# Optimization experiments

Hardware: AMD Instinct MI355X
Metric: run time of the kernel (lower is better)

## Reference

```python
import jax, jax.numpy as jnp
import numpy as np

DIM = 96
RES = (8, 56, 56)
WIN = (8, 7, 7)
SHIFT = (4, 3, 3)
HEADS = (3, 6)
EPS = 1e-5


def _rel_pos_index(wd, wh, ww):
    coords = np.stack(np.meshgrid(np.arange(wd), np.arange(wh), np.arange(ww), indexing='ij'))
    cf = coords.reshape(3, -1)                       # (3, N)
    rel = (cf[:, :, None] - cf[:, None, :]).transpose(1, 2, 0)  # (N, N, 3)
    rel[..., 0] += wd - 1
    rel[..., 1] += wh - 1
    rel[..., 2] += ww - 1
    rel[..., 0] *= (2 * wh - 1) * (2 * ww - 1)
    rel[..., 1] *= (2 * ww - 1)
    return rel.sum(-1)                               # (N, N) int


def _attn_mask(D, H, W, win, shift):
    wd, wh, ww = win
    sd, sh, sw = shift
    img = np.zeros((D, H, W), np.float32)
    cnt = 0
    for ds in (slice(0, -wd), slice(-wd, -sd), slice(-sd, None)):
        for hs in (slice(0, -wh), slice(-wh, -sh), slice(-sh, None)):
            for vs in (slice(0, -ww), slice(-ww, -sw), slice(-sw, None)):
                img[ds, hs, vs] = cnt
                cnt += 1
    m = img.reshape(D // wd, wd, H // wh, wh, W // ww, ww)
    m = m.transpose(0, 2, 4, 1, 3, 5).reshape(-1, wd * wh * ww)   # (nW, N)
    diff = m[:, None, :] - m[:, :, None]
    return np.where(diff != 0, np.float32(-100.0), np.float32(0.0))


def _ln_c(x, w, b):
    # LayerNorm over the channel dim of (B,C,D,H,W)
    mu = x.mean(axis=1, keepdims=True)
    var = ((x - mu) ** 2).mean(axis=1, keepdims=True)
    xn = (x - mu) * jax.lax.rsqrt(var + EPS)
    return xn * w[None, :, None, None, None] + b[None, :, None, None, None]


def _window_partition(x, win):
    B, C, D, H, W = x.shape
    wd, wh, ww = win
    x = x.transpose(0, 2, 3, 4, 1)
    x = x.reshape(B, D // wd, wd, H // wh, wh, W // ww, ww, C)
    x = x.transpose(0, 1, 3, 5, 2, 4, 6, 7)
    return x.reshape(-1, wd * wh * ww, C)            # (B*nW, N, C)


def _window_reverse(w, win, B, D, H, W):
    wd, wh, ww = win
    C = w.shape[-1]
    x = w.reshape(B, D // wd, H // wh, W // ww, wd, wh, ww, C)
    x = x.transpose(0, 1, 4, 2, 5, 3, 6, 7).reshape(B, D, H, W, C)
    return x.transpose(0, 4, 1, 2, 3)


def _win_attn(xw, mask, rel_idx, qkv_w, qkv_b, proj_w, proj_b, rpb, h):
    Bn, N, C = xw.shape
    dh = C // h
    qkv = (xw @ qkv_w.T + qkv_b).reshape(Bn, N, 3, h, dh).transpose(2, 0, 3, 1, 4)
    q, k, v = qkv[0], qkv[1], qkv[2]                 # (Bn, h, N, dh)
    attn = jnp.einsum('bhnd,bhmd->bhnm', q * (dh ** -0.5), k)
    bias = rpb[rel_idx.reshape(-1)].reshape(N, N, h).transpose(2, 0, 1)
    attn = attn + bias[None]
    nW = mask.shape[0]
    attn = (attn.reshape(Bn // nW, nW, h, N, N) + mask[None, :, None]).reshape(Bn, h, N, N)
    attn = jax.nn.softmax(attn, axis=-1)
    out = jnp.einsum('bhnm,bhmd->bhnd', attn, v).transpose(0, 2, 1, 3).reshape(Bn, N, C)
    return out @ proj_w.T + proj_b


def _conv3d(x, w, b, groups=1):
    y = jax.lax.conv_general_dilated(x, w, (1, 1, 1), 'SAME',
                                     dimension_numbers=('NCDHW', 'OIDHW', 'NCDHW'),
                                     feature_group_count=groups)
    return y + b[None, :, None, None, None]


def setup_inputs() -> dict:
    key = jax.random.key(0)
    ks = jax.random.split(key, 16)
    C = DIM
    s = 0.02
    inp = {
        'x': jax.random.normal(ks[0], (2, C, *RES), jnp.float32),
        'ln1_w': jnp.ones((C,), jnp.float32), 'ln1_b': jnp.zeros((C,), jnp.float32),
        'ln2_w': jnp.ones((C,), jnp.float32), 'ln2_b': jnp.zeros((C,), jnp.float32),
        'qkv_w0': jax.random.normal(ks[1], (3 * C, C), jnp.float32) * s,
        'qkv_b0': jnp.zeros((3 * C,), jnp.float32),
        'proj_w0': jax.random.normal(ks[2], (C, C), jnp.float32) * s,
        'proj_b0': jnp.zeros((C,), jnp.float32),
        'rpb0': jax.random.normal(ks[3], (15 * 13 * 13, HEADS[0]), jnp.float32) * s,
        'qkv_w1': jax.random.normal(ks[4], (3 * C, C), jnp.float32) * s,
        'qkv_b1': jnp.zeros((3 * C,), jnp.float32),
        'proj_w1': jax.random.normal(ks[5], (C, C), jnp.float32) * s,
        'proj_b1': jnp.zeros((C,), jnp.float32),
        'rpb1': jax.random.normal(ks[6], (15 * 13 * 13, HEADS[1]), jnp.float32) * s,
        'alpha_attn': jax.random.normal(ks[7], (2,), jnp.float32),
        'conv3_w': jax.random.normal(ks[8], (C, C, 3, 3, 3), jnp.float32) * s,
        'conv3_b': jnp.zeros((C,), jnp.float32),
        'conv1_w': jax.random.normal(ks[9], (C, C, 1, 1, 1), jnp.float32) * s,
        'conv1_b': jnp.zeros((C,), jnp.float32),
        'dw_w': jax.random.normal(ks[10], (C, 1, 3, 3, 3), jnp.float32) * s,
        'dw_b': jnp.zeros((C,), jnp.float32),
        'alpha_ffn': jax.random.normal(ks[11], (4,), jnp.float32),
    }
    return inp


def reference(x, ln1_w, ln1_b, ln2_w, ln2_b,
              qkv_w0, qkv_b0, proj_w0, proj_b0, rpb0,
              qkv_w1, qkv_b1, proj_w1, proj_b1, rpb1,
              alpha_attn, conv3_w, conv3_b, conv1_w, conv1_b, dw_w, dw_b, alpha_ffn):
    B, C, D, H, W = x.shape
    sd, sh, sw = SHIFT
    mask = jnp.asarray(_attn_mask(D, H, W, WIN, SHIFT))     # (nW, N, N), constant
    rel_idx = jnp.asarray(_rel_pos_index(*WIN))             # (N, N), constant

    # --- attention branch (soft NAS mixture) ---
    xn = _ln_c(x, ln1_w, ln1_b)
    shifted = jnp.roll(xn, (-sd, -sh, -sw), axis=(2, 3, 4))
    win = _window_partition(shifted, WIN)
    aw = jax.nn.softmax(alpha_attn)
    a0 = _win_attn(win, mask, rel_idx, qkv_w0, qkv_b0, proj_w0, proj_b0, rpb0, HEADS[0])
    a1 = _win_attn(win, mask, rel_idx, qkv_w1, qkv_b1, proj_w1, proj_b1, rpb1, HEADS[1])
    attn_out = aw[0] * a0 + aw[1] * a1
    xr = _window_reverse(attn_out, WIN, B, D, H, W)
    x_attn = jnp.roll(xr, (sd, sh, sw), axis=(2, 3, 4))
    x1 = x + x_attn                                         # gate=None -> 1.0, drop_path=0

    # --- FFN branch (soft NAS mixture of conv ops) ---
    x2 = _ln_c(x1, ln2_w, ln2_b)
    fw = jax.nn.softmax(alpha_ffn)
    ffn = (fw[0] * _conv3d(x2, conv3_w, conv3_b)
           + fw[1] * _conv3d(x2, conv1_w, conv1_b)
           + fw[2] * _conv3d(x2, dw_w, dw_b, groups=C)
           + fw[3] * x2)
    return x1 + ffn
```

## Files before the change

kernel.cpp:

```cpp
#include <hip/hip_runtime.h>

#define NWIN 128
#define NTOK 392
#define SPAT 25088
#define NELEM 4816896

typedef unsigned short u16t;
typedef unsigned int u32t;
typedef __attribute__((ext_vector_type(8))) short short8;
typedef __attribute__((ext_vector_type(4))) float f32x4;

#define PW 58
#define PHW 3364
#define PSPAT 33640
#define XPAD_U16 6458880
#define WCOMB_N 248832
#define WPROJ_N 18432
#define NTOKTOT 50176
#define LOG2E 1.44269504f

__device__ __forceinline__ unsigned int f2bf(float f) {
  unsigned int u = __float_as_uint(f);
  return (u + 0x7fffu + ((u >> 16) & 1u)) >> 16;
}
__device__ __forceinline__ unsigned int pack2(float a, float b) {
  return f2bf(a) | (f2bf(b) << 16);
}
__device__ __forceinline__ u32t cvtpk(float lo, float hi) {
  u32t r;
  asm("v_cvt_pk_bf16_f32 %0, %1, %2" : "=v"(r) : "v"(lo), "v"(hi));
  return r;
}
__device__ __forceinline__ float exp2v(float x) {
  return __builtin_amdgcn_exp2f(x);
}
__device__ __forceinline__ float bflo(unsigned int u) { return __uint_as_float(u << 16); }

__global__ __launch_bounds__(128)
void k_ln1_win(const float* __restrict__ x, const float* __restrict__ lw,
               const float* __restrict__ lb, u16t* __restrict__ xw) {
  __shared__ float s1[128], s2[128];
  int t = blockIdx.x;
  int win = t / NTOK, n = t % NTOK;
  int b = win >> 6, wrem = win & 63;
  int hwin = wrem >> 3, wwin = wrem & 7;
  int ld = n / 49, r = n % 49, lh = r / 7, lw2 = r % 7;
  int d = (ld + 4) & 7;
  int h = (hwin * 7 + lh + 3) % 56;
  int w = (wwin * 7 + lw2 + 3) % 56;
  size_t base = (size_t)b * 96 * SPAT + d * 3136 + h * 56 + w;
  int c = threadIdx.x;
  float v = (c < 96) ? x[base + (size_t)c * SPAT] : 0.f;
  s1[c] = v; s2[c] = v * v;
  __syncthreads();
  #pragma unroll
  for (int st = 64; st > 0; st >>= 1) {
    if (c < st) { s1[c] += s1[c + st]; s2[c] += s2[c + st]; }
    __syncthreads();
  }
  float mu = s1[0] * (1.f / 96.f);
  float var = s2[0] * (1.f / 96.f) - mu * mu;
  float rs = rsqrtf(var + 1e-5f);
  if (c < 96) xw[(size_t)t * 96 + c] = (u16t)f2bf((v - mu) * rs * lw[c] + lb[c]);
}

__global__ __launch_bounds__(256)
void k_qprep(const float* __restrict__ w0, const float* __restrict__ w1,
             u16t* __restrict__ wq) {
  int e = blockIdx.x * 256 + threadIdx.x;
  if (e >= 2 * 27648) return;
  wq[e] = (u16t)f2bf(e < 27648 ? w0[e] : w1[e - 27648]);
}

template<int DH>
__global__ __launch_bounds__(256)
void k_qkv_mfma(const u16t* __restrict__ xw, const u16t* __restrict__ wq,
                const float* __restrict__ bias, u16t* __restrict__ qkvh) {
  int tid = threadIdx.x;
  int lane = tid & 63, wv = tid >> 6;
  int c = lane & 15, lg = lane >> 4;
  int t = blockIdx.x * 64 + wv * 16 + c;
  const u16t* bp = xw + (size_t)t * 96 + lg * 8;
  short8 bv[3];
  #pragma unroll
  for (int kc = 0; kc < 3; ++kc)
    bv[kc] = *reinterpret_cast<const short8*>(bp + kc * 32);
  f32x4 acc[18];
  #pragma unroll
  for (int f = 0; f < 18; ++f) acc[f] = (f32x4){0.f, 0.f, 0.f, 0.f};
  #pragma unroll
  for (int kc = 0; kc < 3; ++kc) {
    #pragma unroll
    for (int f = 0; f < 18; ++f) {
      short8 av = *reinterpret_cast<const short8*>(
          wq + (size_t)(f * 16 + c) * 96 + kc * 32 + lg * 8);
      acc[f] = __builtin_amdgcn_mfma_f32_16x16x32_bf16(av, bv[kc], acc[f], 0, 0, 0);
    }
  }
  #pragma unroll
  for (int f = 0; f < 18; ++f) {
    int co = f * 16 + lg * 4;
    float4 bb = *reinterpret_cast<const float4*>(bias + co);
    uint2 st = make_uint2(pack2(acc[f][0] + bb.x, acc[f][1] + bb.y),
                          pack2(acc[f][2] + bb.z, acc[f][3] + bb.w));
    int sel = co / 96, rem = co % 96;
    int head = rem / DH, dh = rem % DH;
    *reinterpret_cast<uint2*>(qkvh + (size_t)sel * NTOKTOT * 96
        + (size_t)head * NTOKTOT * DH + (size_t)t * DH + dh) = st;
  }
}

template<int H>
__global__ __launch_bounds__(256)
void k_rprep(const float* __restrict__ rpb, u16t* __restrict__ rpbc) {
  int e = blockIdx.x * 256 + threadIdx.x;
  if (e >= H * 2536) return;
  int h = e / 2536, idx = e % 2536;
  rpbc[e] = (idx < 2535) ? (u16t)f2bf(rpb[idx * H + h] * LOG2E) : (u16t)0;
}

template<int H, int DH>
__global__ __launch_bounds__(512, (DH == 16) ? 6 : 4)
void k_attn_mfma(const u16t* __restrict__ qkvh, const u16t* __restrict__ rpbc,
                 u16t* __restrict__ aout) {
  constexpr float SCALE2 = ((DH == 32) ? 0.17677669529663689f : 0.25f) * LOG2E;
  constexpr float MASKV = -100.f * LOG2E;
  constexpr float THR = 8.f * LOG2E;
  constexpr int NT = DH / 16;
  constexpr int QSPLIT = (DH == 16) ? 1 : 2;
  constexpr int KROW = (DH == 32) ? 32 : 16;
  constexpr int KS_U16 = (DH == 32) ? (416 * 32) : (417 * 16);
  constexpr int BLK = 512;
  __shared__ __align__(16) u16t Ks[KS_U16];
  __shared__ __align__(16) u16t VTs[DH * 424];
  __shared__ u16t rpbs[2536];
  __shared__ u16t Ts[416];
  __shared__ u32t RGp[104];
  __shared__ u32t RGm[26];

  int bid = blockIdx.x;
  int xcd = bid & 7, i = bid >> 3;
  int win = xcd * 16 + (i & 15);
  int hp = i >> 4;
  int head = (DH == 32) ? (hp >> 1) : hp;
  int part = (DH == 32) ? (hp & 1) : 0;
  int wrem = win & 63;
  int hwin = wrem >> 3, wwin = wrem & 7;
  int tid = threadIdx.x;
  int lane = tid & 63, wv = tid >> 6;
  int c = lane & 15, lg = lane >> 4;

  const u16t* qh = qkvh + (size_t)head * NTOKTOT * DH + (size_t)win * NTOK * DH;
  const u16t* kh = qh + (size_t)NTOKTOT * 96;
  const u16t* vh = qh + (size_t)2 * NTOKTOT * 96;
  u16t* ao = aout + (size_t)head * NTOKTOT * DH + (size_t)win * NTOK * DH;

  {
    uint4 z = make_uint4(0u, 0u, 0u, 0u);
    uint4* k4 = (uint4*)Ks;
    for (int i2 = tid; i2 < KS_U16 / 8; i2 += BLK) k4[i2] = z;
    uint4* v4 = (uint4*)VTs;
    for (int i2 = tid; i2 < (DH * 424) / 8; i2 += BLK) v4[i2] = z;
  }
  __syncthreads();
  constexpr int DG = DH / 8;
  for (int u = tid; u < NTOK * DG; u += BLK) {
    int j = u / DG, dg = u % DG;
    uint4 kv = *reinterpret_cast<const uint4*>(kh + (size_t)j * DH + dg * 8);
    int sch = (DH == 32) ? (dg ^ (j & 3)) : (dg ^ ((j & 1) ^ ((j >> 2) & 1)));
    *reinterpret_cast<uint4*>(&Ks[j * KROW + sch * 8]) = kv;
    union { uint4 q; u16t s[8]; } vv;
    vv.q = *reinterpret_cast<const uint4*>(vh + (size_t)j * DH + dg * 8);
    #pragma unroll
    for (int ee = 0; ee < 8; ++ee) VTs[(dg * 8 + ee) * 424 + j] = vv.s[ee];
  }
  for (int i2 = tid; i2 < 2536; i2 += BLK) rpbs[i2] = rpbc[head * 2536 + i2];
  for (int j = tid; j < 416; j += BLK) {
    u16t tv = 0;
    if (j < NTOK) {
      int ld = j / 49, r = j % 49, lh = r / 7, lw = r % 7;
      tv = (u16t)(ld * 169 + lh * 13 + lw);
    }
    Ts[j] = tv;
  }
  for (int j4 = tid; j4 < 104; j4 += BLK) {
    u32t w = 0;
    #pragma unroll
    for (int bb = 0; bb < 4; ++bb) {
      int j = j4 * 4 + bb;
      u32t rg = 255;
      if (j < NTOK) {
        int ld = j / 49, r = j % 49, lh = r / 7, lw = r % 7;
        int hpp = hwin * 7 + lh, wpp = wwin * 7 + lw;
        int rd = (ld < 4) ? 1 : 2;
        int rh = (hpp < 49) ? 0 : ((hpp < 53) ? 1 : 2);
        int rw = (wpp < 49) ? 0 : ((wpp < 53) ? 1 : 2);
        rg = (u32t)(rd * 9 + rh * 3 + rw);
      }
      w |= rg << (8 * bb);
    }
    RGp[j4] = w;
  }
  __syncthreads();
  if (tid < 26) {
    u32t msk = 0;
    #pragma unroll
    for (int j4 = 0; j4 < 4; ++j4) {
      u32t w = RGp[tid * 4 + j4];
      #pragma unroll
      for (int bb = 0; bb < 4; ++bb) {
        u32t rg = (w >> (8 * bb)) & 255u;
        if (rg < 27u) msk |= (1u << rg);
      }
    }
    RGm[tid] = msk;
  }
  __syncthreads();

  constexpr int QBASE = 25 / QSPLIT;
  constexpr int QREM = 25 % QSPLIT;
  int q0 = part * QBASE + ((part < QREM) ? part : QREM);
  int q1 = q0 + QBASE + ((part < QREM) ? 1 : 0);

  for (int qt = q0 + wv; qt < q1; qt += 8) {
    int qtok = qt * 16 + c;
    int qcl = (qtok < NTOK) ? qtok : NTOK - 1;
    int Tq = (int)Ts[qcl] + 1267;
    u32t rgq = (RGp[qcl >> 2] >> ((qcl & 3) * 8)) & 255u;
    u32t qmask = RGm[qt < 25 ? qt : 24];
    short8 bq;
    {
      const u16t* qp = qh + (size_t)qcl * DH;
      union { u32t u[4]; short8 v; } bu;
      #pragma unroll
      for (int i2 = 0; i2 < 4; ++i2) {
        u16t e0 = (DH == 32 || lg < 2) ? qp[lg * 8 + 2 * i2] : (u16t)0;
        u16t e1 = (DH == 32 || lg < 2) ? qp[lg * 8 + 2 * i2 + 1] : (u16t)0;
        bu.u[i2] = (u32t)e0 | ((u32t)e1 << 16);
      }
      bq = bu.v;
    }
    float m = -1e30f, lsum = 0.f;
    f32x4 oacc[NT];
    #pragma unroll
    for (int ot = 0; ot < NT; ++ot) oacc[ot] = (f32x4){0.f, 0.f, 0.f, 0.f};
    int srcl = ((lane >> 4) & 1) * 32 + c;
    #pragma unroll 1
    for (int tt = 0; tt < 13; ++tt) {
      u32t kmask = RGm[2 * tt] | ((2 * tt + 1 < 26) ? RGm[2 * tt + 1] : 0u);
      if ((qmask & kmask) == 0u) continue;
      f32x4 p0, p1;
      #pragma unroll
      for (int half = 0; half < 2; ++half) {
        int t = 2 * tt + half;
        int addr;
        if (DH == 32) {
          addr = (16 * t + c) * 32 + ((lg ^ (c & 3)) * 8);
        } else {
          int fc = (c & 1) ^ ((c >> 2) & 1);
          addr = (lg < 2) ? ((16 * t + c) * 16 + (((lg & 1) ^ fc) * 8)) : (416 * 16);
        }
        short8 av = *reinterpret_cast<const short8*>(&Ks[addr]);
        f32x4 a = (f32x4){0.f, 0.f, 0.f, 0.f};
        a = __builtin_amdgcn_mfma_f32_16x16x32_bf16(av, bq, a, 0, 0, 0);
        int kb = 16 * t + lg * 4;
        const u32t* tsp = reinterpret_cast<const u32t*>(&Ts[kb]);
        u32t tsa = tsp[0], tsb = tsp[1];
        u32t rgw = RGp[4 * t + lg];
        f32x4 p;
        p[0] = a[0] * SCALE2 + bflo((u32t)rpbs[Tq - (int)(tsa & 0xffffu)])
             + ((((rgw      ) & 255u) != rgq) ? MASKV : 0.f);
        p[1] = a[1] * SCALE2 + bflo((u32t)rpbs[Tq - (int)(tsa >> 16)])
             + ((((rgw >>  8) & 255u) != rgq) ? MASKV : 0.f);
        p[2] = a[2] * SCALE2 + bflo((u32t)rpbs[Tq - (int)(tsb & 0xffffu)])
             + ((((rgw >> 16) & 255u) != rgq) ? MASKV : 0.f);
        p[3] = a[3] * SCALE2 + bflo((u32t)rpbs[Tq - (int)(tsb >> 16)])
             + ((((rgw >> 24)        ) != rgq) ? MASKV : 0.f);
        if (half == 0) p0 = p; else p1 = p;
      }
      float pm = fmaxf(fmaxf(fmaxf(p0[0], p0[1]), fmaxf(p0[2], p0[3])),
                       fmaxf(fmaxf(p1[0], p1[1]), fmaxf(p1[2], p1[3])));
      pm = fmaxf(pm, __shfl_xor(pm, 16));
      pm = fmaxf(pm, __shfl_xor(pm, 32));
      bool dead = (pm <= m - 25.f) || (pm <= -90.f);
      if (__all(dead)) continue;
      if (!__all(pm <= m + THR)) {
        float mnew = fmaxf(pm, m);
        float fac = exp2v(m - mnew);
        lsum *= fac;
        #pragma unroll
        for (int ot = 0; ot < NT; ++ot) oacc[ot] *= fac;
        m = mnew;
      }
      #pragma unroll
      for (int j = 0; j < 4; ++j) {
        p0[j] = exp2v(p0[j] - m);
        p1[j] = exp2v(p1[j] - m);
      }
      lsum += p0[0] + p0[1] + p0[2] + p0[3] + p1[0] + p1[1] + p1[2] + p1[3];
      u32t pk0x = cvtpk(p0[0], p0[1]);
      u32t pk0y = cvtpk(p0[2], p0[3]);
      u32t pk1x = cvtpk(p1[0], p1[1]);
      u32t pk1y = cvtpk(p1[2], p1[3]);
      u32t ax = (u32t)__shfl((int)pk0x, srcl),      ay = (u32t)__shfl((int)pk0y, srcl);
      u32t bx = (u32t)__shfl((int)pk0x, srcl + 16), by = (u32t)__shfl((int)pk0y, srcl + 16);
      u32t cx = (u32t)__shfl((int)pk1x, srcl),      cy = (u32t)__shfl((int)pk1y, srcl);
      u32t dx = (u32t)__shfl((int)pk1x, srcl + 16), dy = (u32t)__shfl((int)pk1y, srcl + 16);
      bool hi = (lane & 32) != 0;
      union { u32t u[4]; short8 v; } au;
      au.u[0] = hi ? cx : ax; au.u[1] = hi ? cy : ay;
      au.u[2] = hi ? dx : bx; au.u[3] = hi ? dy : by;
      #pragma unroll
      for (int ot = 0; ot < NT; ++ot) {
        short8 bv = *reinterpret_cast<const short8*>(
            &VTs[(ot * 16 + c) * 424 + 32 * tt + lg * 8]);
        oacc[ot] = __builtin_amdgcn_mfma_f32_16x16x32_bf16(au.v, bv, oacc[ot], 0, 0, 0);
      }
    }
    lsum += __shfl_xor(lsum, 16);
    lsum += __shfl_xor(lsum, 32);
    float inv = 1.f / lsum;
    float invj[4];
    #pragma unroll
    for (int j = 0; j < 4; ++j) invj[j] = __shfl(inv, lg * 4 + j);
    #pragma unroll
    for (int j = 0; j < 4; ++j) {
      int q = qt * 16 + lg * 4 + j;
      if (q < NTOK) {
        #pragma unroll
        for (int ot = 0; ot < NT; ++ot)
          ao[(size_t)q * DH + ot * 16 + c] = (u16t)f2bf(oacc[ot][j] * invj[j]);
      }
    }
  }
}

__global__ __launch_bounds__(256)
void k_pprep(const float* __restrict__ pw0, const float* __restrict__ pb0,
             const float* __restrict__ pw1, const float* __restrict__ pb1,
             const float* __restrict__ alpha,
             u16t* __restrict__ wp, float* __restrict__ bp) {
  int e = blockIdx.x * 256 + threadIdx.x;
  if (e >= WPROJ_N) return;
  float al0 = alpha[0], al1 = alpha[1];
  float m = fmaxf(al0, al1);
  float e0 = expf(al0 - m), e1 = expf(al1 - m);
  float aw0 = e0 / (e0 + e1), aw1 = e1 / (e0 + e1);
  int co = e / 192, k = e % 192;
  float v = (k < 96) ? aw0 * pw0[co * 96 + k] : aw1 * pw1[co * 96 + k - 96];
  wp[e] = (u16t)f2bf(v);
  if (e < 96) bp[e] = aw0 * pb0[e] + aw1 * pb1[e];
}

__global__ __launch_bounds__(64)
void k_proj_mfma(const u16t* __restrict__ a0, const u16t* __restrict__ a1,
                 const u16t* __restrict__ wp, const float* __restrict__ bp,
                 const float* __restrict__ x, float* __restrict__ x1) {
  int lane = threadIdx.x;
  int c = lane & 15, lg = lane >> 4;
  int t = blockIdx.x * 16 + c;
  int win = t / NTOK, n = t % NTOK;
  int b = win >> 6, wrem = win & 63;
  int hwin = wrem >> 3, wwin = wrem & 7;
  int ld = n / 49, r = n % 49, lh = r / 7, lw = r % 7;
  int d = (ld + 4) & 7;
  int h = (hwin * 7 + lh + 3) % 56;
  int w = (wwin * 7 + lw + 3) % 56;
  size_t base = (size_t)b * 96 * SPAT + d * 3136 + h * 56 + w;

  f32x4 acc[6];
  #pragma unroll
  for (int f = 0; f < 6; ++f) acc[f] = (f32x4){0.f, 0.f, 0.f, 0.f};
  #pragma unroll
  for (int kc = 0; kc < 6; ++kc) {
    short8 bv;
    if (kc < 3) {
      bv = *reinterpret_cast<const short8*>(a0 + ((size_t)kc * NTOKTOT + t) * 32 + lg * 8);
    } else {
      int h1 = (kc - 3) * 2 + (lg >> 1);
      bv = *reinterpret_cast<const short8*>(a1 + ((size_t)h1 * NTOKTOT + t) * 16 + (lg & 1) * 8);
    }
    #pragma unroll
    for (int f = 0; f < 6; ++f) {
      short8 av = *reinterpret_cast<const short8*>(wp + (f * 16 + c) * 192 + kc * 32 + lg * 8);
      acc[f] = __builtin_amdgcn_mfma_f32_16x16x32_bf16(av, bv, acc[f], 0, 0, 0);
    }
  }
  #pragma unroll
  for (int f = 0; f < 6; ++f) {
    #pragma unroll
    for (int j = 0; j < 4; ++j) {
      int co = f * 16 + lg * 4 + j;
      size_t idx = base + (size_t)co * SPAT;
      x1[idx] = x[idx] + acc[f][j] + bp[co];
    }
  }
}

__global__ __launch_bounds__(256)
void k_zero(uint4* __restrict__ p, int n) {
  int i = blockIdx.x * 256 + threadIdx.x;
  if (i < n) p[i] = make_uint4(0u, 0u, 0u, 0u);
}

__global__ __launch_bounds__(256)
void k_wprep(const float* __restrict__ c3w, const float* __restrict__ c3b,
             const float* __restrict__ c1w, const float* __restrict__ c1b,
             const float* __restrict__ dww, const float* __restrict__ dwb,
             const float* __restrict__ alpha,
             u16t* __restrict__ wcomb, float* __restrict__ bcomb) {
  int e = blockIdx.x * 256 + threadIdx.x;
  if (e >= WCOMB_N) return;
  float a0 = alpha[0], a1 = alpha[1], a2 = alpha[2], a3 = alpha[3];
  float mx = fmaxf(fmaxf(a0, a1), fmaxf(a2, a3));
  float e0 = expf(a0 - mx), e1 = expf(a1 - mx), e2 = expf(a2 - mx), e3 = expf(a3 - mx);
  float inv = 1.f / (e0 + e1 + e2 + e3);
  float f0 = e0 * inv, f1 = e1 * inv, f2 = e2 * inv, f3 = e3 * inv;
  int ko = e / 9216, rm = e % 9216, co = rm / 96, ci = rm % 96;
  float v = f0 * c3w[(co * 96 + ci) * 27 + ko];
  if (ko == 13) v += f1 * c1w[co * 96 + ci];
  if (ci == co) v += f2 * dww[co * 27 + ko];
  if (ko == 13 && ci == co) v += f3;
  wcomb[e] = (u16t)f2bf(v);
  if (e < 96) bcomb[e] = f0 * c3b[e] + f1 * c1b[e] + f2 * dwb[e];
}

__global__ __launch_bounds__(256)
void k_ln2pad(const float* __restrict__ x1, const float* __restrict__ lw,
              const float* __restrict__ lb, u16t* __restrict__ xpad) {
  int p = blockIdx.x * 256 + threadIdx.x;
  int b = p / SPAT, s = p % SPAT;
  int d = s / 3136, r = s % 3136, h = r / 56, w = r % 56;
  const float* xp = x1 + (size_t)b * 96 * SPAT + s;
  float sum = 0.f, sq = 0.f;
  #pragma unroll 8
  for (int c = 0; c < 96; ++c) {
    float v = xp[(size_t)c * SPAT];
    sum += v; sq += v * v;
  }
  float mu = sum * (1.f / 96.f);
  float var = sq * (1.f / 96.f) - mu * mu;
  float rs = rsqrtf(var + 1e-5f);
  int psp = ((b * 10 + d + 1) * 58 + (h + 1)) * 58 + (w + 1);
  u16t* op = xpad + (size_t)psp * 96;
  #pragma unroll
  for (int g = 0; g < 12; ++g) {
    float v0 = xp[(size_t)(8 * g + 0) * SPAT], v1 = xp[(size_t)(8 * g + 1) * SPAT];
    float v2 = xp[(size_t)(8 * g + 2) * SPAT], v3 = xp[(size_t)(8 * g + 3) * SPAT];
    float v4 = xp[(size_t)(8 * g + 4) * SPAT], v5 = xp[(size_t)(8 * g + 5) * SPAT];
    float v6 = xp[(size_t)(8 * g + 6) * SPAT], v7 = xp[(size_t)(8 * g + 7) * SPAT];
    uint4 st;
    st.x = pack2((v0 - mu) * rs * lw[8*g+0] + lb[8*g+0], (v1 - mu) * rs * lw[8*g+1] + lb[8*g+1]);
    st.y = pack2((v2 - mu) * rs * lw[8*g+2] + lb[8*g+2], (v3 - mu) * rs * lw[8*g+3] + lb[8*g+3]);
    st.z = pack2((v4 - mu) * rs * lw[8*g+4] + lb[8*g+4], (v5 - mu) * rs * lw[8*g+5] + lb[8*g+5]);
    st.w = pack2((v6 - mu) * rs * lw[8*g+6] + lb[8*g+6], (v7 - mu) * rs * lw[8*g+7] + lb[8*g+7]);
    *reinterpret_cast<uint4*>(op + g * 8) = st;
  }
}

__global__ __launch_bounds__(256)
void k_ffn_mfma(const u16t* __restrict__ xpad, const u16t* __restrict__ wcomb,
                const float* __restrict__ bcomb, float* __restrict__ out) {
  __shared__ __align__(16) u16t wls[2][48 * 104];
  int tid = threadIdx.x;
  int lane = tid & 63, wv = tid >> 6;
  int c = lane & 15, kg = lane >> 4;
  int bid = blockIdx.x;
  int coh = bid & 1;
  int sp = bid >> 1;
  int swz = (sp & 7) * 98 + (sp >> 3);
  int m = swz * 64 + wv * 16 + c;
  int b = m / SPAT, r = m % SPAT;
  int d = r / 3136, r2 = r % 3136, h = r2 / 56, w = r2 % 56;
  int psp0 = ((b * 10 + d) * 58 + h) * 58 + w;
  int pbase = psp0 * 96 + kg * 8;
  int obase = b * (96 * SPAT) + r;

  f32x4 acc[3];
  #pragma unroll
  for (int ff = 0; ff < 3; ++ff) acc[ff] = (f32x4){0.f, 0.f, 0.f, 0.f};

  {
    const uint4* src = (const uint4*)(wcomb) + coh * 576;
    for (int e = tid; e < 576; e += 256) {
      uint4 v = src[e];
      int lco = (e * 8) / 96, ci = (e * 8) % 96;
      *reinterpret_cast<uint4*>(&wls[0][lco * 104 + ci]) = v;
    }
  }
  __syncthreads();
  int buf = 0;
  for (int ko = 0; ko < 27; ++ko) {
    int kd = ko / 9, kh = (ko / 3) % 3, kw = ko % 3;
    int tapoff = (kd * PHW + kh * PW + kw) * 96;
    if (ko + 1 < 27) {
      const uint4* src = (const uint4*)(wcomb) + (ko + 1) * 1152 + coh * 576;
      for (int e = tid; e < 576; e += 256) {
        uint4 v = src[e];
        int lco = (e * 8) / 96, ci = (e * 8) % 96;
        *reinterpret_cast<uint4*>(&wls[buf ^ 1][lco * 104 + ci]) = v;
      }
    }
    #pragma unroll
    for (int cc = 0; cc < 3; ++cc) {
      short8 bv = *reinterpret_cast<const short8*>(xpad + pbase + tapoff + cc * 32);
      #pragma unroll
      for (int ff = 0; ff < 3; ++ff) {
        short8 av = *reinterpret_cast<const short8*>(
            &wls[buf][(ff * 16 + c) * 104 + cc * 32 + kg * 8]);
        acc[ff] = __builtin_amdgcn_mfma_f32_16x16x32_bf16(av, bv, acc[ff], 0, 0, 0);
      }
    }
    __syncthreads();
    buf ^= 1;
  }
  #pragma unroll
  for (int ff = 0; ff < 3; ++ff)
    #pragma unroll
    for (int j = 0; j < 4; ++j) {
      int co = coh * 48 + ff * 16 + kg * 4 + j;
      float* o = out + obase + co * SPAT;
      *o = *o + acc[ff][j] + bcomb[co];
    }
}

extern "C" void kernel_launch(void* const* d_in, const int* in_sizes, int n_in,
                              void* d_out, int out_size, void* d_ws, size_t ws_size,
                              hipStream_t stream) {
  (void)in_sizes; (void)n_in; (void)out_size; (void)ws_size;
  const float* x      = (const float*)d_in[0];
  const float* ln1w   = (const float*)d_in[1];
  const float* ln1b   = (const float*)d_in[2];
  const float* ln2w   = (const float*)d_in[3];
  const float* ln2b   = (const float*)d_in[4];
  const float* qkvw0  = (const float*)d_in[5];
  const float* qkvb0  = (const float*)d_in[6];
  const float* projw0 = (const float*)d_in[7];
  const float* projb0 = (const float*)d_in[8];
  const float* rpb0   = (const float*)d_in[9];
  const float* qkvw1  = (const float*)d_in[10];
  const float* qkvb1  = (const float*)d_in[11];
  const float* projw1 = (const float*)d_in[12];
  const float* projb1 = (const float*)d_in[13];
  const float* rpb1   = (const float*)d_in[14];
  const float* aattn  = (const float*)d_in[15];
  const float* c3w    = (const float*)d_in[16];
  const float* c3b    = (const float*)d_in[17];
  const float* c1w    = (const float*)d_in[18];
  const float* c1b    = (const float*)d_in[19];
  const float* dww    = (const float*)d_in[20];
  const float* dwb    = (const float*)d_in[21];
  const float* affn   = (const float*)d_in[22];

  u16t* u    = (u16t*)d_ws;
  u16t* xw   = u;
  u16t* a0   = xw + (size_t)NTOKTOT * 96;
  u16t* a1   = a0 + (size_t)3 * NTOKTOT * 32;
  u16t* qkvh = a1 + (size_t)6 * NTOKTOT * 16;
  u16t* wq   = qkvh + (size_t)3 * NTOKTOT * 96;
  u16t* rpbc0 = wq + 2 * 27648;
  u16t* rpbc1 = rpbc0 + 3 * 2536;
  u16t* xpad  = qkvh;
  u16t* wcomb = xpad + XPAD_U16;
  float* bcomb = (float*)(wcomb + WCOMB_N);
  u16t* wproj = (u16t*)(bcomb + 96);
  float* bproj = (float*)(wproj + WPROJ_N);
  float* x1  = (float*)d_out;

  k_ln1_win<<<NWIN * NTOK, 128, 0, stream>>>(x, ln1w, ln1b, xw);
  k_qprep<<<216, 256, 0, stream>>>(qkvw0, qkvw1, wq);
  k_rprep<3><<<30, 256, 0, stream>>>(rpb0, rpbc0);
  k_rprep<6><<<60, 256, 0, stream>>>(rpb1, rpbc1);
  k_qkv_mfma<32><<<784, 256, 0, stream>>>(xw, wq, qkvb0, qkvh);
  k_attn_mfma<3, 32><<<768, 512, 0, stream>>>(qkvh, rpbc0, a0);
  k_qkv_mfma<16><<<784, 256, 0, stream>>>(xw, wq + 27648, qkvb1, qkvh);
  k_attn_mfma<6, 16><<<768, 512, 0, stream>>>(qkvh, rpbc1, a1);
  k_zero<<<(XPAD_U16 / 8 + 255) / 256, 256, 0, stream>>>((uint4*)xpad, XPAD_U16 / 8);
  k_wprep<<<(WCOMB_N + 255) / 256, 256, 0, stream>>>(c3w, c3b, c1w, c1b, dww, dwb,
                                                     affn, wcomb, bcomb);
  k_pprep<<<(WPROJ_N + 255) / 256, 256, 0, stream>>>(projw0, projb0, projw1, projb1,
                                                     aattn, wproj, bproj);
  k_proj_mfma<<<3136, 64, 0, stream>>>(a0, a1, wproj, bproj, x, x1);
  k_ln2pad<<<196, 256, 0, stream>>>(x1, ln2w, ln2b, xpad);
  k_ffn_mfma<<<1568, 256, 0, stream>>>(xpad, wcomb, bcomb, (float*)d_out);
}
```

Measured before the change: 290.9 us.

## Compute LN1 per spatial position in one thread instead of per-token block

The first LayerNorm plus window partition kernel used one 128-thread block per token, with a shared-memory tree reduction over channels and many barriers. It now assigns one thread per spatial position: the thread loops over the 96 channels with coalesced reads across positions, computes mean and variance in registers, then re-reads the channels and writes the normalized bf16 values as 16-byte vector stores to the shifted window slot. This removes about 50K tiny blocks and their synchronization, at the cost of reading each input twice and launching only 196 blocks, which may underfill the GPU.

```diff
diff --git a/kernel.cpp b/kernel.cpp
--- a/kernel.cpp
+++ b/kernel.cpp
@@ -36,32 +36,41 @@
 }
 __device__ __forceinline__ float bflo(unsigned int u) { return __uint_as_float(u << 16); }
 
-__global__ __launch_bounds__(128)
+__global__ __launch_bounds__(256)
 void k_ln1_win(const float* __restrict__ x, const float* __restrict__ lw,
                const float* __restrict__ lb, u16t* __restrict__ xw) {
-  __shared__ float s1[128], s2[128];
-  int t = blockIdx.x;
-  int win = t / NTOK, n = t % NTOK;
-  int b = win >> 6, wrem = win & 63;
-  int hwin = wrem >> 3, wwin = wrem & 7;
-  int ld = n / 49, r = n % 49, lh = r / 7, lw2 = r % 7;
-  int d = (ld + 4) & 7;
-  int h = (hwin * 7 + lh + 3) % 56;
-  int w = (wwin * 7 + lw2 + 3) % 56;
-  size_t base = (size_t)b * 96 * SPAT + d * 3136 + h * 56 + w;
-  int c = threadIdx.x;
-  float v = (c < 96) ? x[base + (size_t)c * SPAT] : 0.f;
-  s1[c] = v; s2[c] = v * v;
-  __syncthreads();
-  #pragma unroll
-  for (int st = 64; st > 0; st >>= 1) {
-    if (c < st) { s1[c] += s1[c + st]; s2[c] += s2[c + st]; }
-    __syncthreads();
-  }
-  float mu = s1[0] * (1.f / 96.f);
-  float var = s2[0] * (1.f / 96.f) - mu * mu;
+  int p = blockIdx.x * 256 + threadIdx.x;
+  int b = p / SPAT, s = p % SPAT;
+  int d = s / 3136, r = s % 3136, h = r / 56, w = r % 56;
+  const float* xp = x + (size_t)b * 96 * SPAT + s;
+  float sum = 0.f, sq = 0.f;
+  #pragma unroll 8
+  for (int c = 0; c < 96; ++c) {
+    float v = xp[(size_t)c * SPAT];
+    sum += v; sq += v * v;
+  }
+  float mu = sum * (1.f / 96.f);
+  float var = sq * (1.f / 96.f) - mu * mu;
   float rs = rsqrtf(var + 1e-5f);
-  if (c < 96) xw[(size_t)t * 96 + c] = (u16t)f2bf((v - mu) * rs * lw[c] + lb[c]);
+  int ds = (d + 4) & 7;
+  int hs = h - 3; if (hs < 0) hs += 56;
+  int ws = w - 3; if (ws < 0) ws += 56;
+  int win = b * 64 + (hs / 7) * 8 + (ws / 7);
+  int n = ds * 49 + (hs % 7) * 7 + (ws % 7);
+  u16t* op = xw + (size_t)(win * NTOK + n) * 96;
+  #pragma unroll
+  for (int g = 0; g < 12; ++g) {
+    float v0 = xp[(size_t)(8 * g + 0) * SPAT], v1 = xp[(size_t)(8 * g + 1) * SPAT];
+    float v2 = xp[(size_t)(8 * g + 2) * SPAT], v3 = xp[(size_t)(8 * g + 3) * SPAT];
+    float v4 = xp[(size_t)(8 * g + 4) * SPAT], v5 = xp[(size_t)(8 * g + 5) * SPAT];
+    float v6 = xp[(size_t)(8 * g + 6) * SPAT], v7 = xp[(size_t)(8 * g + 7) * SPAT];
+    uint4 st;
+    st.x = pack2((v0 - mu) * rs * lw[8*g+0] + lb[8*g+0], (v1 - mu) * rs * lw[8*g+1] + lb[8*g+1]);
+    st.y = pack2((v2 - mu) * rs * lw[8*g+2] + lb[8*g+2], (v3 - mu) * rs * lw[8*g+3] + lb[8*g+3]);
+    st.z = pack2((v4 - mu) * rs * lw[8*g+4] + lb[8*g+4], (v5 - mu) * rs * lw[8*g+5] + lb[8*g+5]);
+    st.w = pack2((v6 - mu) * rs * lw[8*g+6] + lb[8*g+6], (v7 - mu) * rs * lw[8*g+7] + lb[8*g+7]);
+    *reinterpret_cast<uint4*>(op + g * 8) = st;
+  }
 }
 
 __global__ __launch_bounds__(256)
@@ -567,7 +576,7 @@
   float* bproj = (float*)(wproj + WPROJ_N);
   float* x1  = (float*)d_out;
 
-  k_ln1_win<<<NWIN * NTOK, 128, 0, stream>>>(x, ln1w, ln1b, xw);
+  k_ln1_win<<<196, 256, 0, stream>>>(x, ln1w, ln1b, xw);
   k_qprep<<<216, 256, 0, stream>>>(qkvw0, qkvw1, wq);
   k_rprep<3><<<30, 256, 0, stream>>>(rpb0, rpbc0);
   k_rprep<6><<<60, 256, 0, stream>>>(rpb1, rpbc1);
```

Measured after the change: 271.6 us. 6.7% less time.
